# Optimization experiments

Measured on AMD Instinct MI355X. Metric: run time of the kernel, lower is better.

## Reference

```python
import jax, jax.numpy as jnp
import numpy as np

D_MODEL = 1024
NHEAD = 16
DIM_HEAD = 64
SCALE = DIM_HEAD ** (-0.5)


def setup_inputs() -> dict:
    key = jax.random.key(0)
    ks = jax.random.split(key, 8)
    B, N = 2, 2048
    inner = NHEAD * DIM_HEAD
    s = 0.02
    return {
        "query": jax.random.normal(ks[0], (B, N, D_MODEL), jnp.float32),
        "key": jax.random.normal(ks[1], (B, N, D_MODEL), jnp.float32),
        "value": jax.random.normal(ks[2], (B, N, D_MODEL), jnp.float32),
        "Wq": jax.random.normal(ks[3], (D_MODEL, inner), jnp.float32) * s,
        "Wk": jax.random.normal(ks[4], (D_MODEL, inner), jnp.float32) * s,
        "Wv": jax.random.normal(ks[5], (D_MODEL, inner), jnp.float32) * s,
        "Wo": jax.random.normal(ks[6], (inner, D_MODEL), jnp.float32) * s,
        "bo": jnp.zeros((D_MODEL,), jnp.float32),
    }


def reference(query, key, value, Wq, Wk, Wv, Wo, bo):
    B, Nq, _ = query.shape
    Nk = key.shape[1]
    # projections (no bias), split heads: [B, N, h, d]
    q = (query @ Wq).reshape(B, Nq, NHEAD, DIM_HEAD)
    k = (key @ Wk).reshape(B, Nk, NHEAD, DIM_HEAD)
    v = (value @ Wv).reshape(B, Nk, NHEAD, DIM_HEAD)
    # scores [B, h, Nq, Nk]
    sim = jnp.einsum('bihd,bjhd->bhij', q, k) * SCALE
    attn = jax.nn.softmax(sim, axis=-1)  # dropout p=0.0 -> identity
    out = jnp.einsum('bhij,bjhd->bihd', attn, v).reshape(B, Nq, NHEAD * DIM_HEAD)
    return out @ Wo + bo
```

## Files before the change

### kernel.cpp

```cpp
#include <hip/hip_runtime.h>
#include <stdint.h>

typedef __attribute__((ext_vector_type(8))) short short8;
typedef __attribute__((ext_vector_type(8))) unsigned short ushort8;
typedef __attribute__((ext_vector_type(4))) unsigned short ushort4v;
typedef __attribute__((ext_vector_type(4))) float float4v;

#define D_MODEL 1024
#define NHEAD 16
#define DIM_HEAD 64
#define BATCH 2
#define SEQ 2048
#define BH (BATCH*NHEAD)
#define MROWS (BATCH*SEQ)
#define MK ((size_t)MROWS * D_MODEL)

__device__ __forceinline__ unsigned short f2bf(float f) {
  union { float f; unsigned u; } v; v.f = f;
  unsigned r = v.u + 0x7fffu + ((v.u >> 16) & 1u);
  return (unsigned short)(r >> 16);
}
__device__ __forceinline__ unsigned short f2bf_fast(float f) {
  union { float f; unsigned u; } v; v.f = f;
  return (unsigned short)((v.u + 0x8000u) >> 16);
}

__device__ __forceinline__ float fexp2(float x) {
#if __has_builtin(__builtin_amdgcn_exp2f)
  return __builtin_amdgcn_exp2f(x);
#else
  return exp2f(x);
#endif
}

__device__ __forceinline__ void gld16(const unsigned short* g, unsigned short* l) {
  __builtin_amdgcn_global_load_lds(
      (const __attribute__((address_space(1))) unsigned int*)g,
      (__attribute__((address_space(3))) unsigned int*)l, 16, 0, 0);
}

__global__ __launch_bounds__(256) void prep_kernel(const float* __restrict__ q,
    const float* __restrict__ k, const float* __restrict__ v,
    unsigned short* __restrict__ Xbf,
    const float* __restrict__ W0, const float* __restrict__ W1,
    const float* __restrict__ W2, const float* __restrict__ W3,
    unsigned short* __restrict__ WT) {
  if (blockIdx.y < 3) {
    const float* src = (blockIdx.y == 0) ? q : (blockIdx.y == 1) ? k : v;
    unsigned short* dst = Xbf + (size_t)blockIdx.y * MK;
    size_t idx = ((size_t)blockIdx.x * 256 + threadIdx.x) * 8;
    float4v a = *(const float4v*)(src + idx);
    float4v b = *(const float4v*)(src + idx + 4);
    ushort8 o;
    o[0] = f2bf(a[0]); o[1] = f2bf(a[1]); o[2] = f2bf(a[2]); o[3] = f2bf(a[3]);
    o[4] = f2bf(b[0]); o[5] = f2bf(b[1]); o[6] = f2bf(b[2]); o[7] = f2bf(b[3]);
    *(ushort8*)(dst + idx) = o;
    return;
  }
  __shared__ float tile[32][33];
  const int z = blockIdx.x >> 9;
  const float* W = (z == 0) ? W0 : (z == 1) ? W1 : (z == 2) ? W2 : W3;
  const float scale = (z == 0) ? 0.18033688f : 1.0f;
  unsigned short* dst = WT + ((size_t)z << 20);
  int tx = threadIdx.x & 31, ty = threadIdx.x >> 5;
#pragma unroll
  for (int rep = 0; rep < 2; rep++) {
    int tl = (blockIdx.x & 511) * 2 + rep;
    int bn = (tl & 31) * 32;
    int bk = (tl >> 5) * 32;
#pragma unroll
    for (int i = 0; i < 4; i++)
      tile[ty + i*8][tx] = W[(size_t)(bk + ty + i*8) * D_MODEL + bn + tx];
    __syncthreads();
#pragma unroll
    for (int i = 0; i < 4; i++)
      dst[(size_t)(bn + ty + i*8) * D_MODEL + bk + tx] = f2bf(tile[tx][ty + i*8] * scale);
    __syncthreads();
  }
}

__global__ __launch_bounds__(256, 3) void proj_kernel(const unsigned short* __restrict__ Xbf,
    const unsigned short* __restrict__ WT0, unsigned short* __restrict__ Y0) {
  __shared__ unsigned short Al[128*64];
  __shared__ unsigned short Bl[128*64];
  const int z = blockIdx.z;
  const unsigned short* A  = Xbf + (size_t)z * MK;
  const unsigned short* BT = WT0 + ((size_t)z << 20);
  unsigned short* Y = Y0 + (size_t)z * MK;
  const int m0 = blockIdx.x * 128, n0 = blockIdx.y * 128;
  const int t = threadIdx.x;
  const int lane = t & 63, w = t >> 6, quad = lane >> 4, lid = lane & 15;
  const int wm = w & 1, wn = w >> 1;
  const int r8 = lane >> 3, c8 = (lane & 7) * 8;

  float4v acc[4][4];
#pragma unroll
  for (int i = 0; i < 4; i++)
#pragma unroll
    for (int j = 0; j < 4; j++) acc[i][j] = (float4v)0.0f;

  for (int k0 = 0; k0 < D_MODEL; k0 += 64) {
#pragma unroll
    for (int p = 0; p < 4; p++) {
      int seg = w*4 + p;
      gld16(A  + (size_t)(m0 + seg*8 + r8) * D_MODEL + k0 + c8, &Al[seg*8*64]);
      gld16(BT + (size_t)(n0 + seg*8 + r8) * D_MODEL + k0 + c8, &Bl[seg*8*64]);
    }
    __syncthreads();
#pragma unroll
    for (int kst = 0; kst < 2; kst++) {
      short8 af[4], bfr[4];
#pragma unroll
      for (int i = 0; i < 4; i++)
        af[i] = *(const short8*)&Al[(wm*64 + i*16 + lid)*64 + kst*32 + quad*8];
#pragma unroll
      for (int j = 0; j < 4; j++)
        bfr[j] = *(const short8*)&Bl[(wn*64 + j*16 + lid)*64 + kst*32 + quad*8];
#pragma unroll
      for (int i = 0; i < 4; i++)
#pragma unroll
        for (int j = 0; j < 4; j++)
          acc[i][j] = __builtin_amdgcn_mfma_f32_16x16x32_bf16(af[i], bfr[j], acc[i][j], 0, 0, 0);
    }
    __syncthreads();
  }
  if (z == 2) {
#pragma unroll
    for (int i = 0; i < 4; i++) {
      int row = m0 + wm*64 + i*16 + quad*4;
      int b_ = row >> 11;
      int n_ = row & 2047;
      int nblk = n_ & ~63;
      int ebase = ((i >> 1) << 5) | (quad << 3) | ((i & 1) << 2);
#pragma unroll
      for (int j = 0; j < 4; j++) {
        int col = n0 + wn*64 + j*16 + lid;
        ushort4v pk;
#pragma unroll
        for (int r = 0; r < 4; r++) pk[r] = f2bf_fast(acc[i][j][r]);
        *(ushort4v*)(Y + ((size_t)((b_*NHEAD + (col >> 6))*DIM_HEAD + (col & 63)))*SEQ
                       + nblk + ebase) = pk;
      }
    }
    return;
  }
#pragma unroll
  for (int i = 0; i < 4; i++)
#pragma unroll
    for (int j = 0; j < 4; j++)
#pragma unroll
      for (int r = 0; r < 4; r++) {
        int row = m0 + wm*64 + i*16 + quad*4 + r;
        int col = n0 + wn*64 + j*16 + lid;
        Y[(size_t)row * D_MODEL + col] = f2bf_fast(acc[i][j][r]);
      }
}

__global__ __launch_bounds__(256, 3) void outproj_kernel(const unsigned short* __restrict__ A,
    const unsigned short* __restrict__ WT, const float* __restrict__ bias,
    float* __restrict__ out) {
  __shared__ unsigned short Al[64*64];
  __shared__ unsigned short Bl[128*64];
  const int m0 = blockIdx.x * 64, n0 = blockIdx.y * 128;
  const int t = threadIdx.x;
  const int lane = t & 63, w = t >> 6, quad = lane >> 4, lid = lane & 15;
  const int wm = w & 1, wn = w >> 1;
  const int r8 = lane >> 3, c8 = (lane & 7) * 8;

  float4v acc[2][4];
#pragma unroll
  for (int i = 0; i < 2; i++)
#pragma unroll
    for (int j = 0; j < 4; j++) acc[i][j] = (float4v)0.0f;

  for (int k0 = 0; k0 < D_MODEL; k0 += 64) {
#pragma unroll
    for (int p = 0; p < 2; p++) {
      int seg = w*2 + p;
      gld16(A + (size_t)(m0 + seg*8 + r8) * D_MODEL + k0 + c8, &Al[seg*8*64]);
    }
#pragma unroll
    for (int p = 0; p < 4; p++) {
      int seg = w*4 + p;
      gld16(WT + (size_t)(n0 + seg*8 + r8) * D_MODEL + k0 + c8, &Bl[seg*8*64]);
    }
    __syncthreads();
#pragma unroll
    for (int kst = 0; kst < 2; kst++) {
      short8 af[2], bfr[4];
#pragma unroll
      for (int i = 0; i < 2; i++)
        af[i] = *(const short8*)&Al[(wm*32 + i*16 + lid)*64 + kst*32 + quad*8];
#pragma unroll
      for (int j = 0; j < 4; j++)
        bfr[j] = *(const short8*)&Bl[(wn*64 + j*16 + lid)*64 + kst*32 + quad*8];
#pragma unroll
      for (int i = 0; i < 2; i++)
#pragma unroll
        for (int j = 0; j < 4; j++)
          acc[i][j] = __builtin_amdgcn_mfma_f32_16x16x32_bf16(af[i], bfr[j], acc[i][j], 0, 0, 0);
    }
    __syncthreads();
  }
#pragma unroll
  for (int i = 0; i < 2; i++)
#pragma unroll
    for (int j = 0; j < 4; j++)
#pragma unroll
      for (int r = 0; r < 4; r++) {
        int row = m0 + wm*32 + i*16 + quad*4 + r;
        int col = n0 + wn*64 + j*16 + lid;
        out[(size_t)row * D_MODEL + col] = acc[i][j][r] + bias[col];
      }
}

#define QB 128
#define KB 64
#define FSTR 72
#define NT (SEQ/KB)

__global__ __launch_bounds__(256, 2) void flash_kernel(const unsigned short* __restrict__ Q,
    const unsigned short* __restrict__ K, const unsigned short* __restrict__ VT,
    unsigned short* __restrict__ O) {
  __shared__ unsigned short Kl[2][KB][FSTR];
  __shared__ unsigned short Vt[2][DIM_HEAD][FSTR];

  const int bh = blockIdx.x;
  const int b = bh >> 4, h = bh & 15;
  const int q0 = blockIdx.y * QB;
  const int t = threadIdx.x;
  const int lane = t & 63, w = t >> 6, quad = lane >> 4, lid = lane & 15;
  const int prow = t >> 3, pc = (t & 7) * 8;

  const unsigned short* Kbase = K + ((size_t)(b*SEQ)*NHEAD + h)*DIM_HEAD;
  const unsigned short* Vbase = VT + (size_t)bh*DIM_HEAD*SEQ;

  short8 qf[2][2];
#pragma unroll
  for (int st = 0; st < 2; st++)
#pragma unroll
    for (int kst = 0; kst < 2; kst++)
      qf[st][kst] = *(const short8*)(Q +
          ((size_t)((b*SEQ + q0 + w*32 + st*16 + lid)*NHEAD + h))*DIM_HEAD + kst*32 + quad*8);

  float4v o[2][4];
#pragma unroll
  for (int st = 0; st < 2; st++)
#pragma unroll
    for (int i = 0; i < 4; i++) o[st][i] = (float4v)0.0f;
  float ps[2] = {0.0f, 0.0f};

  auto LOADT = [&](int kb, ushort8* kr, ushort8* vr) {
#pragma unroll
    for (int p = 0; p < 2; p++) {
      int row = p*32 + prow;
      kr[p] = *(const ushort8*)(Kbase + (size_t)(kb + row) * D_MODEL + pc);
      vr[p] = *(const ushort8*)(Vbase + (size_t)row * SEQ + kb + pc);
    }
  };
  auto COMMIT = [&](int bi, const ushort8* kr, const ushort8* vr) {
#pragma unroll
    for (int p = 0; p < 2; p++) {
      int row = p*32 + prow;
      *(ushort8*)&Kl[bi][row][pc] = kr[p];
      *(ushort8*)&Vt[bi][row][pc] = vr[p];
    }
  };
  auto STEP = [&](int bi) {
    float4v s[2][4];
#pragma unroll
    for (int st = 0; st < 2; st++)
#pragma unroll
      for (int n = 0; n < 4; n++) s[st][n] = (float4v)0.0f;
    __builtin_amdgcn_s_setprio(1);
#pragma unroll
    for (int kst = 0; kst < 2; kst++)
#pragma unroll
      for (int n = 0; n < 4; n++) {
        short8 kf = *(const short8*)&Kl[bi][n*16 + lid][kst*32 + quad*8];
        s[0][n] = __builtin_amdgcn_mfma_f32_16x16x32_bf16(kf, qf[0][kst], s[0][n], 0, 0, 0);
        s[1][n] = __builtin_amdgcn_mfma_f32_16x16x32_bf16(kf, qf[1][kst], s[1][n], 0, 0, 0);
      }
    __builtin_amdgcn_s_setprio(0);
    union PF { unsigned u[4]; short8 v8; };
    PF pf0[2], pf1[2];
#pragma unroll
    for (int n = 0; n < 4; n++) {
      float p0[4], p1[4];
#pragma unroll
      for (int r = 0; r < 4; r++) {
        p0[r] = fexp2(s[0][n][r]);
        p1[r] = fexp2(s[1][n][r]);
        ps[0] += p0[r]; ps[1] += p1[r];
      }
      const int hh = n >> 1, bb = 2*(n & 1);
      asm("v_cvt_pk_bf16_f32 %0, %1, %2" : "=v"(pf0[hh].u[bb+0]) : "v"(p0[0]), "v"(p0[1]));
      asm("v_cvt_pk_bf16_f32 %0, %1, %2" : "=v"(pf0[hh].u[bb+1]) : "v"(p0[2]), "v"(p0[3]));
      asm("v_cvt_pk_bf16_f32 %0, %1, %2" : "=v"(pf1[hh].u[bb+0]) : "v"(p1[0]), "v"(p1[1]));
      asm("v_cvt_pk_bf16_f32 %0, %1, %2" : "=v"(pf1[hh].u[bb+1]) : "v"(p1[2]), "v"(p1[3]));
    }
    __builtin_amdgcn_s_setprio(1);
#pragma unroll
    for (int kst = 0; kst < 2; kst++)
#pragma unroll
      for (int i = 0; i < 4; i++) {
        short8 vf = *(const short8*)&Vt[bi][i*16 + lid][kst*32 + quad*8];
        o[0][i] = __builtin_amdgcn_mfma_f32_16x16x32_bf16(pf0[kst].v8, vf, o[0][i], 0, 0, 0);
        o[1][i] = __builtin_amdgcn_mfma_f32_16x16x32_bf16(pf1[kst].v8, vf, o[1][i], 0, 0, 0);
      }
    __builtin_amdgcn_s_setprio(0);
  };

  ushort8 krA[2], vrA[2], krB[2], vrB[2];
  LOADT(0, krA, vrA);
  LOADT(KB, krB, vrB);
  COMMIT(0, krA, vrA);
  __syncthreads();

  for (int i = 0; i < NT; i += 2) {
    if (i + 2 < NT) LOADT((i + 2)*KB, krA, vrA);
    STEP(0);
    if (i + 1 < NT) COMMIT(1, krB, vrB);
    __syncthreads();
    if (i + 3 < NT) LOADT((i + 3)*KB, krB, vrB);
    STEP(1);
    if (i + 2 < NT) COMMIT(0, krA, vrA);
    __syncthreads();
  }

  float dr[2][4];
#pragma unroll
  for (int st = 0; st < 2; st++) {
    float v = ps[st];
    v += __shfl_xor(v, 16);
    v += __shfl_xor(v, 32);
    v = 1.0f / v;
#pragma unroll
    for (int r = 0; r < 4; r++) dr[st][r] = __shfl(v, quad*4 + r);
  }
#pragma unroll
  for (int st = 0; st < 2; st++)
#pragma unroll
    for (int i = 0; i < 4; i++)
#pragma unroll
      for (int r = 0; r < 4; r++) {
        int q = q0 + w*32 + st*16 + quad*4 + r;
        O[((size_t)((b*SEQ + q)*NHEAD + h))*DIM_HEAD + i*16 + lid] =
          f2bf(o[st][i][r] * dr[st][r]);
      }
}

extern "C" void kernel_launch(void* const* d_in, const int* in_sizes, int n_in,
                              void* d_out, int out_size, void* d_ws, size_t ws_size,
                              hipStream_t stream) {
  const float* query = (const float*)d_in[0];
  const float* key_  = (const float*)d_in[1];
  const float* value = (const float*)d_in[2];
  const float* Wq = (const float*)d_in[3];
  const float* Wk = (const float*)d_in[4];
  const float* Wv = (const float*)d_in[5];
  const float* Wo = (const float*)d_in[6];
  const float* bo = (const float*)d_in[7];
  float* out = (float*)d_out;

  char* ws = (char*)d_ws;
  unsigned short* WqT = (unsigned short*)(ws + (0ll  << 20));
  unsigned short* WoT = (unsigned short*)(ws + (6ll  << 20));
  unsigned short* Xbf = (unsigned short*)(ws + (8ll  << 20));
  unsigned short* Qb  = (unsigned short*)(ws + (32ll << 20));
  unsigned short* Kb  = Qb + MK;
  unsigned short* VT  = Qb + 2*MK;
  unsigned short* Ob  = (unsigned short*)(ws + (16ll << 20));

  dim3 tb(256);
  dim3 pr(2048, 4);
  hipLaunchKernelGGL(prep_kernel, pr, tb, 0, stream,
                     query, key_, value, Xbf, Wq, Wk, Wv, Wo, WqT);

  dim3 pg(MROWS/128, D_MODEL/128, 3);
  hipLaunchKernelGGL(proj_kernel, pg, tb, 0, stream, Xbf, WqT, Qb);

  dim3 fg(BH, SEQ/QB);
  hipLaunchKernelGGL(flash_kernel, fg, tb, 0, stream, Qb, Kb, VT, Ob);

  dim3 og(MROWS/64, D_MODEL/128);
  hipLaunchKernelGGL(outproj_kernel, og, tb, 0, stream, Ob, WoT, bo, out);
}
```

Before: 205.4 us.

## Fuse fp32-to-bf16 activation conversion into projection GEMM tile loads

Removes the standalone pass that converted query/key/value to bf16 in workspace. The projection kernel now reads fp32 activations directly, converts them in registers, and writes them to LDS. The weight transpose becomes its own smaller kernel with one tile per block. This saves a full write and re-read of the bf16 activation copies. In exchange, each projection block reads fp32 (twice the bytes) for every N-tile, about 8 tiles per row, and the async global-to-LDS path for A becomes synchronous register loads, which may stall the GEMM.

New measurement: 212.1 us. +3.2%, slower.

```diff
diff --git a/kernel.cpp b/kernel.cpp
--- a/kernel.cpp
+++ b/kernel.cpp
@@ -39,52 +39,33 @@
       (__attribute__((address_space(3))) unsigned int*)l, 16, 0, 0);
 }
 
-__global__ __launch_bounds__(256) void prep_kernel(const float* __restrict__ q,
-    const float* __restrict__ k, const float* __restrict__ v,
-    unsigned short* __restrict__ Xbf,
-    const float* __restrict__ W0, const float* __restrict__ W1,
-    const float* __restrict__ W2, const float* __restrict__ W3,
-    unsigned short* __restrict__ WT) {
-  if (blockIdx.y < 3) {
-    const float* src = (blockIdx.y == 0) ? q : (blockIdx.y == 1) ? k : v;
-    unsigned short* dst = Xbf + (size_t)blockIdx.y * MK;
-    size_t idx = ((size_t)blockIdx.x * 256 + threadIdx.x) * 8;
-    float4v a = *(const float4v*)(src + idx);
-    float4v b = *(const float4v*)(src + idx + 4);
-    ushort8 o;
-    o[0] = f2bf(a[0]); o[1] = f2bf(a[1]); o[2] = f2bf(a[2]); o[3] = f2bf(a[3]);
-    o[4] = f2bf(b[0]); o[5] = f2bf(b[1]); o[6] = f2bf(b[2]); o[7] = f2bf(b[3]);
-    *(ushort8*)(dst + idx) = o;
-    return;
-  }
+__global__ __launch_bounds__(256) void wtrans_kernel(const float* __restrict__ W0,
+    const float* __restrict__ W1, const float* __restrict__ W2,
+    const float* __restrict__ W3, unsigned short* __restrict__ WT) {
   __shared__ float tile[32][33];
-  const int z = blockIdx.x >> 9;
+  const int z = blockIdx.z;
   const float* W = (z == 0) ? W0 : (z == 1) ? W1 : (z == 2) ? W2 : W3;
   const float scale = (z == 0) ? 0.18033688f : 1.0f;
   unsigned short* dst = WT + ((size_t)z << 20);
+  int bn = blockIdx.x * 32;
+  int bk = blockIdx.y * 32;
   int tx = threadIdx.x & 31, ty = threadIdx.x >> 5;
 #pragma unroll
-  for (int rep = 0; rep < 2; rep++) {
-    int tl = (blockIdx.x & 511) * 2 + rep;
-    int bn = (tl & 31) * 32;
-    int bk = (tl >> 5) * 32;
-#pragma unroll
-    for (int i = 0; i < 4; i++)
-      tile[ty + i*8][tx] = W[(size_t)(bk + ty + i*8) * D_MODEL + bn + tx];
-    __syncthreads();
-#pragma unroll
-    for (int i = 0; i < 4; i++)
-      dst[(size_t)(bn + ty + i*8) * D_MODEL + bk + tx] = f2bf(tile[tx][ty + i*8] * scale);
-    __syncthreads();
-  }
-}
-
-__global__ __launch_bounds__(256, 3) void proj_kernel(const unsigned short* __restrict__ Xbf,
+  for (int i = 0; i < 4; i++)
+    tile[ty + i*8][tx] = W[(size_t)(bk + ty + i*8) * D_MODEL + bn + tx];
+  __syncthreads();
+#pragma unroll
+  for (int i = 0; i < 4; i++)
+    dst[(size_t)(bn + ty + i*8) * D_MODEL + bk + tx] = f2bf(tile[tx][ty + i*8] * scale);
+}
+
+__global__ __launch_bounds__(256, 3) void proj_kernel(const float* __restrict__ Xq,
+    const float* __restrict__ Xk, const float* __restrict__ Xv,
     const unsigned short* __restrict__ WT0, unsigned short* __restrict__ Y0) {
   __shared__ unsigned short Al[128*64];
   __shared__ unsigned short Bl[128*64];
   const int z = blockIdx.z;
-  const unsigned short* A  = Xbf + (size_t)z * MK;
+  const float* X = (z == 0) ? Xq : (z == 1) ? Xk : Xv;
   const unsigned short* BT = WT0 + ((size_t)z << 20);
   unsigned short* Y = Y0 + (size_t)z * MK;
   const int m0 = blockIdx.x * 128, n0 = blockIdx.y * 128;
@@ -103,8 +84,18 @@
 #pragma unroll
     for (int p = 0; p < 4; p++) {
       int seg = w*4 + p;
-      gld16(A  + (size_t)(m0 + seg*8 + r8) * D_MODEL + k0 + c8, &Al[seg*8*64]);
       gld16(BT + (size_t)(n0 + seg*8 + r8) * D_MODEL + k0 + c8, &Bl[seg*8*64]);
+    }
+#pragma unroll
+    for (int p = 0; p < 4; p++) {
+      int seg = w*4 + p;
+      const float* src = X + (size_t)(m0 + seg*8 + r8) * D_MODEL + k0 + c8;
+      float4v a = *(const float4v*)src;
+      float4v b = *(const float4v*)(src + 4);
+      ushort8 o;
+      o[0] = f2bf(a[0]); o[1] = f2bf(a[1]); o[2] = f2bf(a[2]); o[3] = f2bf(a[3]);
+      o[4] = f2bf(b[0]); o[5] = f2bf(b[1]); o[6] = f2bf(b[2]); o[7] = f2bf(b[3]);
+      *(ushort8*)&Al[seg*8*64 + lane*8] = o;
     }
     __syncthreads();
 #pragma unroll
@@ -366,19 +357,17 @@
   char* ws = (char*)d_ws;
   unsigned short* WqT = (unsigned short*)(ws + (0ll  << 20));
   unsigned short* WoT = (unsigned short*)(ws + (6ll  << 20));
-  unsigned short* Xbf = (unsigned short*)(ws + (8ll  << 20));
   unsigned short* Qb  = (unsigned short*)(ws + (32ll << 20));
   unsigned short* Kb  = Qb + MK;
   unsigned short* VT  = Qb + 2*MK;
   unsigned short* Ob  = (unsigned short*)(ws + (16ll << 20));
 
   dim3 tb(256);
-  dim3 pr(2048, 4);
-  hipLaunchKernelGGL(prep_kernel, pr, tb, 0, stream,
-                     query, key_, value, Xbf, Wq, Wk, Wv, Wo, WqT);
+  dim3 wg(32, 32, 4);
+  hipLaunchKernelGGL(wtrans_kernel, wg, tb, 0, stream, Wq, Wk, Wv, Wo, WqT);
 
   dim3 pg(MROWS/128, D_MODEL/128, 3);
-  hipLaunchKernelGGL(proj_kernel, pg, tb, 0, stream, Xbf, WqT, Qb);
+  hipLaunchKernelGGL(proj_kernel, pg, tb, 0, stream, query, key_, value, WqT, Qb);
 
   dim3 fg(BH, SEQ/QB);
   hipLaunchKernelGGL(flash_kernel, fg, tb, 0, stream, Qb, Kb, VT, Ob);
```

## Double-buffer LDS tiles in projection and output GEMMs to overlap loads

Applied to the files above, without the earlier changes.

Both bf16 MFMA GEMM kernels (the QKV projection and the output projection) now keep two LDS buffers for the A and B tiles. The loads for the next k-tile are issued before computing on the current one, which halves the barriers per iteration and hides global-to-LDS latency behind MFMA work. This doubles LDS use per block, so the projection kernel's launch bound drops from 3 to 2 blocks per CU, trading occupancy for overlap.

Result: slower. 224.1 us (+9.1%).

```diff
diff --git a/kernel.cpp b/kernel.cpp
--- a/kernel.cpp
+++ b/kernel.cpp
@@ -79,10 +79,10 @@
   }
 }
 
-__global__ __launch_bounds__(256, 3) void proj_kernel(const unsigned short* __restrict__ Xbf,
+__global__ __launch_bounds__(256, 2) void proj_kernel(const unsigned short* __restrict__ Xbf,
     const unsigned short* __restrict__ WT0, unsigned short* __restrict__ Y0) {
-  __shared__ unsigned short Al[128*64];
-  __shared__ unsigned short Bl[128*64];
+  __shared__ unsigned short Al[2][128*64];
+  __shared__ unsigned short Bl[2][128*64];
   const int z = blockIdx.z;
   const unsigned short* A  = Xbf + (size_t)z * MK;
   const unsigned short* BT = WT0 + ((size_t)z << 20);
@@ -99,23 +99,29 @@
 #pragma unroll
     for (int j = 0; j < 4; j++) acc[i][j] = (float4v)0.0f;
 
-  for (int k0 = 0; k0 < D_MODEL; k0 += 64) {
+  auto STAGE = [&](int bi, int k0) {
 #pragma unroll
     for (int p = 0; p < 4; p++) {
       int seg = w*4 + p;
-      gld16(A  + (size_t)(m0 + seg*8 + r8) * D_MODEL + k0 + c8, &Al[seg*8*64]);
-      gld16(BT + (size_t)(n0 + seg*8 + r8) * D_MODEL + k0 + c8, &Bl[seg*8*64]);
-    }
-    __syncthreads();
+      gld16(A  + (size_t)(m0 + seg*8 + r8) * D_MODEL + k0 + c8, &Al[bi][seg*8*64]);
+      gld16(BT + (size_t)(n0 + seg*8 + r8) * D_MODEL + k0 + c8, &Bl[bi][seg*8*64]);
+    }
+  };
+
+  STAGE(0, 0);
+  __syncthreads();
+  int bi = 0;
+  for (int k0 = 0; k0 < D_MODEL; k0 += 64) {
+    if (k0 + 64 < D_MODEL) STAGE(bi ^ 1, k0 + 64);
 #pragma unroll
     for (int kst = 0; kst < 2; kst++) {
       short8 af[4], bfr[4];
 #pragma unroll
       for (int i = 0; i < 4; i++)
-        af[i] = *(const short8*)&Al[(wm*64 + i*16 + lid)*64 + kst*32 + quad*8];
+        af[i] = *(const short8*)&Al[bi][(wm*64 + i*16 + lid)*64 + kst*32 + quad*8];
 #pragma unroll
       for (int j = 0; j < 4; j++)
-        bfr[j] = *(const short8*)&Bl[(wn*64 + j*16 + lid)*64 + kst*32 + quad*8];
+        bfr[j] = *(const short8*)&Bl[bi][(wn*64 + j*16 + lid)*64 + kst*32 + quad*8];
 #pragma unroll
       for (int i = 0; i < 4; i++)
 #pragma unroll
@@ -123,6 +129,7 @@
           acc[i][j] = __builtin_amdgcn_mfma_f32_16x16x32_bf16(af[i], bfr[j], acc[i][j], 0, 0, 0);
     }
     __syncthreads();
+    bi ^= 1;
   }
   if (z == 2) {
 #pragma unroll
@@ -159,8 +166,8 @@
 __global__ __launch_bounds__(256, 3) void outproj_kernel(const unsigned short* __restrict__ A,
     const unsigned short* __restrict__ WT, const float* __restrict__ bias,
     float* __restrict__ out) {
-  __shared__ unsigned short Al[64*64];
-  __shared__ unsigned short Bl[128*64];
+  __shared__ unsigned short Al[2][64*64];
+  __shared__ unsigned short Bl[2][128*64];
   const int m0 = blockIdx.x * 64, n0 = blockIdx.y * 128;
   const int t = threadIdx.x;
   const int lane = t & 63, w = t >> 6, quad = lane >> 4, lid = lane & 15;
@@ -173,27 +180,33 @@
 #pragma unroll
     for (int j = 0; j < 4; j++) acc[i][j] = (float4v)0.0f;
 
-  for (int k0 = 0; k0 < D_MODEL; k0 += 64) {
+  auto STAGE = [&](int bi, int k0) {
 #pragma unroll
     for (int p = 0; p < 2; p++) {
       int seg = w*2 + p;
-      gld16(A + (size_t)(m0 + seg*8 + r8) * D_MODEL + k0 + c8, &Al[seg*8*64]);
+      gld16(A + (size_t)(m0 + seg*8 + r8) * D_MODEL + k0 + c8, &Al[bi][seg*8*64]);
     }
 #pragma unroll
     for (int p = 0; p < 4; p++) {
       int seg = w*4 + p;
-      gld16(WT + (size_t)(n0 + seg*8 + r8) * D_MODEL + k0 + c8, &Bl[seg*8*64]);
-    }
-    __syncthreads();
+      gld16(WT + (size_t)(n0 + seg*8 + r8) * D_MODEL + k0 + c8, &Bl[bi][seg*8*64]);
+    }
+  };
+
+  STAGE(0, 0);
+  __syncthreads();
+  int bi = 0;
+  for (int k0 = 0; k0 < D_MODEL; k0 += 64) {
+    if (k0 + 64 < D_MODEL) STAGE(bi ^ 1, k0 + 64);
 #pragma unroll
     for (int kst = 0; kst < 2; kst++) {
       short8 af[2], bfr[4];
 #pragma unroll
       for (int i = 0; i < 2; i++)
-        af[i] = *(const short8*)&Al[(wm*32 + i*16 + lid)*64 + kst*32 + quad*8];
+        af[i] = *(const short8*)&Al[bi][(wm*32 + i*16 + lid)*64 + kst*32 + quad*8];
 #pragma unroll
       for (int j = 0; j < 4; j++)
-        bfr[j] = *(const short8*)&Bl[(wn*64 + j*16 + lid)*64 + kst*32 + quad*8];
+        bfr[j] = *(const short8*)&Bl[bi][(wn*64 + j*16 + lid)*64 + kst*32 + quad*8];
 #pragma unroll
       for (int i = 0; i < 2; i++)
 #pragma unroll
@@ -201,6 +214,7 @@
           acc[i][j] = __builtin_amdgcn_mfma_f32_16x16x32_bf16(af[i], bfr[j], acc[i][j], 0, 0, 0);
     }
     __syncthreads();
+    bi ^= 1;
   }
 #pragma unroll
   for (int i = 0; i < 2; i++)
```
